# Optimization experiments

Hardware: AMD Instinct MI355X
Metric: run time of the kernel (lower is better)

Reference implementation:

```python
import jax, jax.numpy as jnp
import numpy as np

B, N, D = 2048, 512, 128

def mexican_hat(z):
    z2 = z * z
    return (1.0 - z2) * jnp.exp(-0.5 * z2)

def setup_inputs() -> dict:
    key = jax.random.key(0)
    k1, k2 = jax.random.split(key)
    x = jax.random.normal(k1, (B, D), dtype=jnp.float32)
    bias = jax.random.normal(k2, (N, D), dtype=jnp.float32)
    scale = jnp.ones((N, D), dtype=jnp.float32)
    return {"x": x, "bias": bias, "scale": scale}

def reference(x, bias, scale):
    # z: (B, N, D) via broadcast of (B,1,D) against (N,D)
    z = (x[:, None, :] - bias) / scale
    psi = mexican_hat(z)
    h = jnp.prod(psi, axis=2)  # (B, N)
    return h
```

## Files before the change

kernel.cpp:

```cpp
#include <hip/hip_runtime.h>

#define DD 128

typedef float v2f __attribute__((ext_vector_type(2)));
typedef float v4f __attribute__((ext_vector_type(4)));
typedef float v8f __attribute__((ext_vector_type(8)));

#define UPD2(P, S, XX, AA, CC)                                   \
    {                                                            \
        v2f z  = __builtin_elementwise_fma((XX), (AA), (CC));    \
        v2f zz = z * z;                                          \
        P = __builtin_elementwise_fma(-zz, P, P);                \
        S += zz;                                                 \
    }

#define UPD8(P, S, XV)                                           \
    {                                                            \
        UPD2(P, S, (XV).lo.lo, a0.lo, c0.lo);                    \
        UPD2(P, S, (XV).lo.hi, a0.hi, c0.hi);                    \
        UPD2(P, S, (XV).hi.lo, a1.lo, c1.lo);                    \
        UPD2(P, S, (XV).hi.hi, a1.hi, c1.hi);                    \
    }

__global__ __launch_bounds__(512, 4)
void wavelet_prod_kernel(const float* __restrict__ x,
                         const float* __restrict__ bias,
                         const float* __restrict__ scale,
                         float* __restrict__ out,
                         int B, int N)
{
    __shared__ v4f a_s[64 * 32];
    __shared__ v4f c_s[64 * 32];

    const int tid  = threadIdx.x;
    const int lane = tid & 63;
    const int wave = tid >> 6;

    const int n0 = blockIdx.x * 64;
    const int bb = blockIdx.y * 64;

    {
        const v4f* b4 = (const v4f*)(bias  + (size_t)n0 * DD);
        const v4f* s4 = (const v4f*)(scale + (size_t)n0 * DD);
        #pragma unroll
        for (int k = 0; k < 4; ++k) {
            int flat = tid + k * 512;
            int r = flat >> 5;
            int q = flat & 31;
            v4f sv = s4[flat];
            v4f bv = b4[flat];
            v4f av, cv;
            av.x = __builtin_amdgcn_rcpf(sv.x);
            av.y = __builtin_amdgcn_rcpf(sv.y);
            av.z = __builtin_amdgcn_rcpf(sv.z);
            av.w = __builtin_amdgcn_rcpf(sv.w);
            cv = -bv * av;
            int dst = r * 32 + (q ^ (r & 7));
            a_s[dst] = av;
            c_s[dst] = cv;
        }
    }
    __syncthreads();

    const int b0 = __builtin_amdgcn_readfirstlane(bb + wave * 8);
    const v8f* xr8 = (const v8f*)(x + (size_t)b0 * DD);

    const v4f* arow = a_s + lane * 32;
    const v4f* crow = c_s + lane * 32;
    const int sw = lane & 7;

    v2f p0 = {1.f, 1.f}, p1 = {1.f, 1.f}, p2 = {1.f, 1.f}, p3 = {1.f, 1.f};
    v2f p4 = {1.f, 1.f}, p5 = {1.f, 1.f}, p6 = {1.f, 1.f}, p7 = {1.f, 1.f};
    v2f s0 = {0.f, 0.f}, s1 = {0.f, 0.f}, s2 = {0.f, 0.f}, s3 = {0.f, 0.f};
    v2f s4v = {0.f, 0.f}, s5 = {0.f, 0.f}, s6 = {0.f, 0.f}, s7 = {0.f, 0.f};

    const float kexp = -0.7213475204444817f;

    #pragma unroll
    for (int w = 0; w < 4; ++w) {
        #pragma unroll
        for (int h = 0; h < 4; ++h) {
            const int q0 = w * 8 + h * 2;
            const int sl0 = q0 ^ sw;
            const int sl1 = (q0 + 1) ^ sw;
            v4f a0 = arow[sl0], c0 = crow[sl0];
            v4f a1 = arow[sl1], c1 = crow[sl1];
            const int xi = w * 4 + h;
            {
                v8f xA0 = xr8[0 * 16 + xi];
                v8f xA1 = xr8[1 * 16 + xi];
                v8f xA2 = xr8[2 * 16 + xi];
                v8f xA3 = xr8[3 * 16 + xi];
                UPD8(p0, s0, xA0);
                UPD8(p1, s1, xA1);
                UPD8(p2, s2, xA2);
                UPD8(p3, s3, xA3);
            }
            {
                v8f xB0 = xr8[4 * 16 + xi];
                v8f xB1 = xr8[5 * 16 + xi];
                v8f xB2 = xr8[6 * 16 + xi];
                v8f xB3 = xr8[7 * 16 + xi];
                UPD8(p4, s4v, xB0);
                UPD8(p5, s5, xB1);
                UPD8(p6, s6, xB2);
                UPD8(p7, s7, xB3);
            }
        }
        p0.x = p0.x * p0.y * __builtin_amdgcn_exp2f((s0.x + s0.y) * kexp);
        p0.y = 1.f; s0 = (v2f){0.f, 0.f};
        p1.x = p1.x * p1.y * __builtin_amdgcn_exp2f((s1.x + s1.y) * kexp);
        p1.y = 1.f; s1 = (v2f){0.f, 0.f};
        p2.x = p2.x * p2.y * __builtin_amdgcn_exp2f((s2.x + s2.y) * kexp);
        p2.y = 1.f; s2 = (v2f){0.f, 0.f};
        p3.x = p3.x * p3.y * __builtin_amdgcn_exp2f((s3.x + s3.y) * kexp);
        p3.y = 1.f; s3 = (v2f){0.f, 0.f};
        p4.x = p4.x * p4.y * __builtin_amdgcn_exp2f((s4v.x + s4v.y) * kexp);
        p4.y = 1.f; s4v = (v2f){0.f, 0.f};
        p5.x = p5.x * p5.y * __builtin_amdgcn_exp2f((s5.x + s5.y) * kexp);
        p5.y = 1.f; s5 = (v2f){0.f, 0.f};
        p6.x = p6.x * p6.y * __builtin_amdgcn_exp2f((s6.x + s6.y) * kexp);
        p6.y = 1.f; s6 = (v2f){0.f, 0.f};
        p7.x = p7.x * p7.y * __builtin_amdgcn_exp2f((s7.x + s7.y) * kexp);
        p7.y = 1.f; s7 = (v2f){0.f, 0.f};
    }

    float* o = out + (size_t)b0 * N + n0 + lane;
    o[0 * N] = p0.x;
    o[1 * N] = p1.x;
    o[2 * N] = p2.x;
    o[3 * N] = p3.x;
    o[4 * N] = p4.x;
    o[5 * N] = p5.x;
    o[6 * N] = p6.x;
    o[7 * N] = p7.x;
}

extern "C" void kernel_launch(void* const* d_in, const int* in_sizes, int n_in,
                              void* d_out, int out_size, void* d_ws, size_t ws_size,
                              hipStream_t stream)
{
    const float* x     = (const float*)d_in[0];
    const float* bias  = (const float*)d_in[1];
    const float* scale = (const float*)d_in[2];
    float* out = (float*)d_out;

    const int B = in_sizes[0] / DD;
    const int N = in_sizes[1] / DD;

    dim3 grid(N / 64, B / 64);
    wavelet_prod_kernel<<<grid, 512, 0, stream>>>(x, bias, scale, out, B, N);
}
```

Before: 18.07 us.

## Halve bias tile per block and split wave lanes across two x row groups

```diff
diff --git a/kernel.cpp b/kernel.cpp
--- a/kernel.cpp
+++ b/kernel.cpp
@@ -29,21 +29,23 @@
                          float* __restrict__ out,
                          int B, int N)
 {
-    __shared__ v4f a_s[64 * 32];
-    __shared__ v4f c_s[64 * 32];
+    __shared__ v4f a_s[32 * 32];
+    __shared__ v4f c_s[32 * 32];
 
     const int tid  = threadIdx.x;
     const int lane = tid & 63;
     const int wave = tid >> 6;
+    const int ncol = lane & 31;
+    const int half = lane >> 5;
 
-    const int n0 = blockIdx.x * 64;
+    const int n0 = blockIdx.x * 32;
     const int bb = blockIdx.y * 64;
 
     {
         const v4f* b4 = (const v4f*)(bias  + (size_t)n0 * DD);
         const v4f* s4 = (const v4f*)(scale + (size_t)n0 * DD);
         #pragma unroll
-        for (int k = 0; k < 4; ++k) {
+        for (int k = 0; k < 2; ++k) {
             int flat = tid + k * 512;
             int r = flat >> 5;
             int q = flat & 31;
@@ -62,17 +64,15 @@
     }
     __syncthreads();
 
-    const int b0 = __builtin_amdgcn_readfirstlane(bb + wave * 8);
-    const v8f* xr8 = (const v8f*)(x + (size_t)b0 * DD);
+    const int r0 = bb + wave * 8 + half * 4;
+    const v8f* xr8 = (const v8f*)(x + (size_t)r0 * DD);
 
-    const v4f* arow = a_s + lane * 32;
-    const v4f* crow = c_s + lane * 32;
-    const int sw = lane & 7;
+    const v4f* arow = a_s + ncol * 32;
+    const v4f* crow = c_s + ncol * 32;
+    const int sw = ncol & 7;
 
     v2f p0 = {1.f, 1.f}, p1 = {1.f, 1.f}, p2 = {1.f, 1.f}, p3 = {1.f, 1.f};
-    v2f p4 = {1.f, 1.f}, p5 = {1.f, 1.f}, p6 = {1.f, 1.f}, p7 = {1.f, 1.f};
     v2f s0 = {0.f, 0.f}, s1 = {0.f, 0.f}, s2 = {0.f, 0.f}, s3 = {0.f, 0.f};
-    v2f s4v = {0.f, 0.f}, s5 = {0.f, 0.f}, s6 = {0.f, 0.f}, s7 = {0.f, 0.f};
 
     const float kexp = -0.7213475204444817f;
 
@@ -86,26 +86,14 @@
             v4f a0 = arow[sl0], c0 = crow[sl0];
             v4f a1 = arow[sl1], c1 = crow[sl1];
             const int xi = w * 4 + h;
-            {
-                v8f xA0 = xr8[0 * 16 + xi];
-                v8f xA1 = xr8[1 * 16 + xi];
-                v8f xA2 = xr8[2 * 16 + xi];
-                v8f xA3 = xr8[3 * 16 + xi];
-                UPD8(p0, s0, xA0);
-                UPD8(p1, s1, xA1);
-                UPD8(p2, s2, xA2);
-                UPD8(p3, s3, xA3);
-            }
-            {
-                v8f xB0 = xr8[4 * 16 + xi];
-                v8f xB1 = xr8[5 * 16 + xi];
-                v8f xB2 = xr8[6 * 16 + xi];
-                v8f xB3 = xr8[7 * 16 + xi];
-                UPD8(p4, s4v, xB0);
-                UPD8(p5, s5, xB1);
-                UPD8(p6, s6, xB2);
-                UPD8(p7, s7, xB3);
-            }
+            v8f x0 = xr8[0 * 16 + xi];
+            v8f x1 = xr8[1 * 16 + xi];
+            v8f x2 = xr8[2 * 16 + xi];
+            v8f x3 = xr8[3 * 16 + xi];
+            UPD8(p0, s0, x0);
+            UPD8(p1, s1, x1);
+            UPD8(p2, s2, x2);
+            UPD8(p3, s3, x3);
         }
         p0.x = p0.x * p0.y * __builtin_amdgcn_exp2f((s0.x + s0.y) * kexp);
         p0.y = 1.f; s0 = (v2f){0.f, 0.f};
@@ -115,25 +103,13 @@
         p2.y = 1.f; s2 = (v2f){0.f, 0.f};
         p3.x = p3.x * p3.y * __builtin_amdgcn_exp2f((s3.x + s3.y) * kexp);
         p3.y = 1.f; s3 = (v2f){0.f, 0.f};
-        p4.x = p4.x * p4.y * __builtin_amdgcn_exp2f((s4v.x + s4v.y) * kexp);
-        p4.y = 1.f; s4v = (v2f){0.f, 0.f};
-        p5.x = p5.x * p5.y * __builtin_amdgcn_exp2f((s5.x + s5.y) * kexp);
-        p5.y = 1.f; s5 = (v2f){0.f, 0.f};
-        p6.x = p6.x * p6.y * __builtin_amdgcn_exp2f((s6.x + s6.y) * kexp);
-        p6.y = 1.f; s6 = (v2f){0.f, 0.f};
-        p7.x = p7.x * p7.y * __builtin_amdgcn_exp2f((s7.x + s7.y) * kexp);
-        p7.y = 1.f; s7 = (v2f){0.f, 0.f};
     }
 
-    float* o = out + (size_t)b0 * N + n0 + lane;
+    float* o = out + (size_t)r0 * N + n0 + ncol;
     o[0 * N] = p0.x;
     o[1 * N] = p1.x;
     o[2 * N] = p2.x;
     o[3 * N] = p3.x;
-    o[4 * N] = p4.x;
-    o[5 * N] = p5.x;
-    o[6 * N] = p6.x;
-    o[7 * N] = p7.x;
 }
 
 extern "C" void kernel_launch(void* const* d_in, const int* in_sizes, int n_in,
@@ -148,6 +124,6 @@
     const int B = in_sizes[0] / DD;
     const int N = in_sizes[1] / DD;
 
-    dim3 grid(N / 64, B / 64);
+    dim3 grid(N / 32, B / 64);
     wavelet_prod_kernel<<<grid, 512, 0, stream>>>(x, bias, scale, out, B, N);
 }
```

After: 21.78 us. +20.5%, slower.

## Split D reduction across two wave halves with LDS product combine

Applied to the files above, without the earlier changes.

```diff
diff --git a/kernel.cpp b/kernel.cpp
--- a/kernel.cpp
+++ b/kernel.cpp
@@ -22,7 +22,7 @@
         UPD2(P, S, (XV).hi.hi, a1.hi, c1.hi);                    \
     }
 
-__global__ __launch_bounds__(512, 4)
+__global__ __launch_bounds__(1024, 4)
 void wavelet_prod_kernel(const float* __restrict__ x,
                          const float* __restrict__ bias,
                          const float* __restrict__ scale,
@@ -31,10 +31,13 @@
 {
     __shared__ v4f a_s[64 * 32];
     __shared__ v4f c_s[64 * 32];
+    __shared__ float comb[8][512];
 
     const int tid  = threadIdx.x;
     const int lane = tid & 63;
     const int wave = tid >> 6;
+    const int w8   = wave & 7;
+    const int dh   = wave >> 3;
 
     const int n0 = blockIdx.x * 64;
     const int bb = blockIdx.y * 64;
@@ -43,8 +46,8 @@
         const v4f* b4 = (const v4f*)(bias  + (size_t)n0 * DD);
         const v4f* s4 = (const v4f*)(scale + (size_t)n0 * DD);
         #pragma unroll
-        for (int k = 0; k < 4; ++k) {
-            int flat = tid + k * 512;
+        for (int k = 0; k < 2; ++k) {
+            int flat = tid + k * 1024;
             int r = flat >> 5;
             int q = flat & 31;
             v4f sv = s4[flat];
@@ -62,12 +65,13 @@
     }
     __syncthreads();
 
-    const int b0 = __builtin_amdgcn_readfirstlane(bb + wave * 8);
-    const v8f* xr8 = (const v8f*)(x + (size_t)b0 * DD);
+    const int b0 = __builtin_amdgcn_readfirstlane(bb + w8 * 8);
+    const v8f* xr8 = (const v8f*)(x + (size_t)b0 * DD) + dh * 8;
 
     const v4f* arow = a_s + lane * 32;
     const v4f* crow = c_s + lane * 32;
-    const int sw = lane & 7;
+    const int sw    = lane & 7;
+    const int qbase = dh * 16;
 
     v2f p0 = {1.f, 1.f}, p1 = {1.f, 1.f}, p2 = {1.f, 1.f}, p3 = {1.f, 1.f};
     v2f p4 = {1.f, 1.f}, p5 = {1.f, 1.f}, p6 = {1.f, 1.f}, p7 = {1.f, 1.f};
@@ -77,10 +81,10 @@
     const float kexp = -0.7213475204444817f;
 
     #pragma unroll
-    for (int w = 0; w < 4; ++w) {
+    for (int w = 0; w < 2; ++w) {
         #pragma unroll
         for (int h = 0; h < 4; ++h) {
-            const int q0 = w * 8 + h * 2;
+            const int q0  = qbase + w * 8 + h * 2;
             const int sl0 = q0 ^ sw;
             const int sl1 = (q0 + 1) ^ sw;
             v4f a0 = arow[sl0], c0 = crow[sl0];
@@ -125,15 +129,29 @@
         p7.y = 1.f; s7 = (v2f){0.f, 0.f};
     }
 
-    float* o = out + (size_t)b0 * N + n0 + lane;
-    o[0 * N] = p0.x;
-    o[1 * N] = p1.x;
-    o[2 * N] = p2.x;
-    o[3 * N] = p3.x;
-    o[4 * N] = p4.x;
-    o[5 * N] = p5.x;
-    o[6 * N] = p6.x;
-    o[7 * N] = p7.x;
+    if (dh == 1) {
+        const int pid = tid - 512;
+        comb[0][pid] = p0.x;
+        comb[1][pid] = p1.x;
+        comb[2][pid] = p2.x;
+        comb[3][pid] = p3.x;
+        comb[4][pid] = p4.x;
+        comb[5][pid] = p5.x;
+        comb[6][pid] = p6.x;
+        comb[7][pid] = p7.x;
+    }
+    __syncthreads();
+    if (dh == 0) {
+        float* o = out + (size_t)b0 * N + n0 + lane;
+        o[0 * N] = p0.x * comb[0][tid];
+        o[1 * N] = p1.x * comb[1][tid];
+        o[2 * N] = p2.x * comb[2][tid];
+        o[3 * N] = p3.x * comb[3][tid];
+        o[4 * N] = p4.x * comb[4][tid];
+        o[5 * N] = p5.x * comb[5][tid];
+        o[6 * N] = p6.x * comb[6][tid];
+        o[7 * N] = p7.x * comb[7][tid];
+    }
 }
 
 extern "C" void kernel_launch(void* const* d_in, const int* in_sizes, int n_in,
@@ -149,5 +167,5 @@
     const int N = in_sizes[1] / DD;
 
     dim3 grid(N / 64, B / 64);
-    wavelet_prod_kernel<<<grid, 512, 0, stream>>>(x, bias, scale, out, B, N);
+    wavelet_prod_kernel<<<grid, 1024, 0, stream>>>(x, bias, scale, out, B, N);
 }
```

Measured after the change: 30.33 us. 1.68x slower.
